# Optimization experiments

Measured on AMD Instinct MI355X. Metric: run time of the kernel, lower is better.

Reference implementation:

```python
import jax, jax.numpy as jnp
import numpy as np

N_FFT = 1024
FREQ = N_FFT // 2 + 1          # 513
FRAMES = 256
WIN_MIN = 10.0                 # max(1, n_fft//100)
WIN_MAX = 1024.0               # n_fft
HOP_MIN = 1.0
HOP_MAX = 256.0
EPS = 1e-12
SIG_LEN = int(HOP_MAX) * FRAMES + N_FFT  # 66560


def setup_inputs() -> dict:
    key = jax.random.key(0)
    k1, k2, k3 = jax.random.split(key, 3)
    x = jax.random.normal(k1, (4, SIG_LEN), dtype=jnp.float32)
    raw_win_length = jax.random.normal(k2, (FREQ,), dtype=jnp.float32)
    raw_hop_length = jax.random.normal(k3, (1,), dtype=jnp.float32)
    return {"x": x, "raw_win_length": raw_win_length, "raw_hop_length": raw_hop_length}


def reference(x, raw_win_length, raw_hop_length):
    B, L = x.shape
    dt = x.dtype
    # sigmoid reparameterization (matches logit init in __init__)
    hop = HOP_MIN + jax.nn.sigmoid(raw_hop_length[0]) * (HOP_MAX - HOP_MIN)      # scalar
    theta = WIN_MIN + jax.nn.sigmoid(raw_win_length) * (WIN_MAX - WIN_MIN)

    # fractional frame positions: integer floor for gather, differentiable frac
    t = jnp.arange(FRAMES, dtype=dt)
    pos = jnp.clip(t * hop, 0.0, float(L - N_FFT))                               # [T]
    idx_floor = jnp.floor(pos).astype(jnp.int32)                                 # [T] (non-diff)
    idx_frac = pos - idx_floor.astype(dt)                                        # [T] (diff: d/dhop = t)

    # unfold: frames[b,t,n] = x[b, idx_floor[t] + n]
    n = jnp.arange(N_FFT)
    frames = x[:, idx_floor[:, None] + n[None, :]]                               # [B,T,N]

    # fractionally-shifted, per-frequency-length hann window: [F,T,N]
    nf = n.astype(dt)
    d = nf[None, :] - (N_FFT - 1) / 2.0 - idx_frac[:, None]                      # [T,N] offset from true center
    th = theta[:, None, None]                                                    # [F,1,1]
    w = jnp.where(jnp.abs(d)[None] <= th / 2.0,
                  0.5 + 0.5 * jnp.cos(2.0 * jnp.pi * d[None] / th),
                  0.0)                                                           # [F,T,N]

    # direct DFT (window varies per freq bin -> no FFT possible)
    k = jnp.arange(FREQ, dtype=dt)
    ang = 2.0 * jnp.pi * k[:, None] * nf[None, :] / N_FFT                        # [F,N]
    re = jnp.einsum('btn,ftn,fn->bft', frames, w, jnp.cos(ang))
    im = -jnp.einsum('btn,ftn,fn->bft', frames, w, jnp.sin(ang))
    stft = jax.lax.complex(re, im)                                               # [B,F,T]
    spec = jnp.abs(stft) + EPS                                                   # magnitude_power = 1
    return spec, stft
```

## Files before the change

kernel.cpp:

```cpp
#include <hip/hip_runtime.h>
#include <math.h>

#define NFFT   1024
#define FREQ   513
#define FRAMES 256
#define SIGLEN 66560
#define NB     4
#define BFT    (NB * FREQ * FRAMES)
#define NWAVE  8
#define NTHR   (64 * NWAVE)
#define NCHUNK 9
#define UNITS  (NCHUNK * FRAMES)

__global__ __launch_bounds__(1024)
void dstft_perm(const float* __restrict__ raw_win, int* __restrict__ perm)
{
    __shared__ float th[FREQ];
    const int tid = threadIdx.x;
    if (tid < FREQ)
        th[tid] = 10.0f + 1014.0f / (1.0f + expf(-raw_win[tid]));
    __syncthreads();
    if (tid < FREQ) {
        const float ti = th[tid];
        int r = 0;
        for (int j = 0; j < FREQ; ++j) {
            const float tj = th[j];
            r += (tj > ti) || (tj == ti && j < tid);
        }
        perm[r] = tid;
    }
}

__device__ __forceinline__ float sigmoid_f32(float v)
{
    if (v >= 0.0f) {
        return 1.0f / (1.0f + expf(-v));
    } else {
        const float e = expf(v);
        return e / (1.0f + e);
    }
}

__device__ __forceinline__ float rfl_f32(float v)
{
    return __int_as_float(__builtin_amdgcn_readfirstlane(__float_as_int(v)));
}

__global__ __launch_bounds__(NTHR)
void dstft_main(const float* __restrict__ x,
                const float* __restrict__ raw_win,
                const float* __restrict__ raw_hop,
                const int* __restrict__ perm,
                float* __restrict__ out, int out_size, int stft_mode)
{
    const int tid  = threadIdx.x;
    const int lane = tid & 63;
    const int q    = tid >> 6;

    __shared__ __align__(16) unsigned char smem[NWAVE * 64 * 9 * 4];
    float4* xlds = reinterpret_cast<float4*>(smem);
    float (*part)[64][9] = reinterpret_cast<float (*)[64][9]>(smem);

    const int u     = (int)blockIdx.x;
    const int chunk = u >> 8;
    const int t     = u & 255;
    const int spos  = chunk * 64 + lane;
    const bool active = (spos < FREQ);

    int f = 0;
    if (active) {
        f = perm ? perm[spos] : spos;
        f = (f < 0) ? 0 : ((f > FREQ - 1) ? (FREQ - 1) : f);
    }
    const float theta = active
        ? (10.0f + sigmoid_f32(raw_win[f]) * 1014.0f)
        : 10.0f;

    float tmaxv = theta;
#pragma unroll
    for (int s = 32; s; s >>= 1)
        tmaxv = fmaxf(tmaxv, __shfl_xor(tmaxv, s, 64));
    const float tmax = rfl_f32(tmaxv);

    const float hop = 1.0f + sigmoid_f32(raw_hop[0]) * 255.0f;
    float pos = (float)t * hop;
    pos = fminf(fmaxf(pos, 0.0f), 65536.0f);
    const float fl   = floorf(pos);
    const int   base = __builtin_amdgcn_readfirstlane((int)fl);
    const float c    = rfl_f32(511.5f + (pos - fl));

    int lo = (int)floorf(c - 0.5f * tmax);
    int hi = (int)ceilf (c + 0.5f * tmax);
    lo = lo > 0 ? lo : 0;
    hi = hi < (NFFT - 1) ? hi : (NFFT - 1);
    int cnt = hi - lo + 1;
    cnt = cnt < 0 ? 0 : (cnt > NFFT ? NFFT : cnt);
    lo  = __builtin_amdgcn_readfirstlane(lo);
    cnt = __builtin_amdgcn_readfirstlane(cnt);

    for (int n = lo + tid; n < lo + cnt; n += NTHR) {
        float4 v;
        v.x = x[base + n];
        v.y = x[base + n + SIGLEN];
        v.z = x[base + n + 2 * SIGLEN];
        v.w = x[base + n + 3 * SIGLEN];
        xlds[n - lo] = v;
    }
    __syncthreads();

    const int s0     = lo + (cnt * q) / NWAVE;
    const int s1     = lo + (cnt * (q + 1)) / NWAVE;
    const int segcnt = s1 - s0;

    const float invth = 1.0f / theta;
    float r = ((float)s0 - c) * invth;

    const float sdr = (float)f * (1.0f / 1024.0f);
    const float cd  = __builtin_amdgcn_cosf(sdr);
    const float sd  = __builtin_amdgcn_sinf(sdr);
    int m0 = (f * s0) & (NFFT - 1);
    m0 = (m0 >= 512) ? (m0 - 1024) : m0;
    const float p0 = (float)m0 * (1.0f / 1024.0f);
    float ca = __builtin_amdgcn_cosf(p0);
    float sa = __builtin_amdgcn_sinf(p0);

    float re0 = 0.f, re1 = 0.f, re2 = 0.f, re3 = 0.f;
    float sm0 = 0.f, sm1 = 0.f, sm2 = 0.f, sm3 = 0.f;

    const float4* __restrict__ xp = &xlds[s0 - lo];
#pragma unroll 4
    for (int i = 0; i < segcnt; ++i) {
        const float rc = __builtin_amdgcn_fmed3f(r, -0.5f, 0.5f);
        const float w  = fmaf(0.5f, __builtin_amdgcn_cosf(rc), 0.5f);
        const float wc  = w * ca;
        const float wsn = w * sa;
        const float4 v = xp[i];
        re0 = fmaf(v.x, wc, re0);  sm0 = fmaf(v.x, wsn, sm0);
        re1 = fmaf(v.y, wc, re1);  sm1 = fmaf(v.y, wsn, sm1);
        re2 = fmaf(v.z, wc, re2);  sm2 = fmaf(v.z, wsn, sm2);
        re3 = fmaf(v.w, wc, re3);  sm3 = fmaf(v.w, wsn, sm3);
        const float nca = fmaf(ca, cd, -(sa * sd));
        const float nsa = fmaf(sa, cd,   ca * sd);
        ca = nca; sa = nsa;
        r += invth;
    }

    __syncthreads();
    part[q][lane][0] = re0;  part[q][lane][1] = re1;
    part[q][lane][2] = re2;  part[q][lane][3] = re3;
    part[q][lane][4] = sm0;  part[q][lane][5] = sm1;
    part[q][lane][6] = sm2;  part[q][lane][7] = sm3;
    __syncthreads();

    if (tid < 256 && active) {
        const int b = tid >> 6;
        float res = 0.f, sms = 0.f;
#pragma unroll
        for (int p = 0; p < NWAVE; ++p) {
            res += part[p][lane][b];
            sms += part[p][lane][4 + b];
        }
        const float re = res;
        const float im = -sms;
        const int idx = b * (FREQ * FRAMES) + f * FRAMES + t;
        if (idx < out_size)
            out[idx] = sqrtf(fmaf(re, re, im * im)) + 1e-12f;
        if (stft_mode == 2) {
            if (BFT + 2 * idx + 1 < out_size) {
                out[BFT + 2 * idx]     = re;
                out[BFT + 2 * idx + 1] = im;
            }
        } else {
            if (BFT + idx < out_size)
                out[BFT + idx] = re;
        }
    }
}

extern "C" void kernel_launch(void* const* d_in, const int* in_sizes, int n_in,
                              void* d_out, int out_size, void* d_ws, size_t ws_size,
                              hipStream_t stream)
{
    const float* x       = (const float*)d_in[0];
    const float* raw_win = (const float*)d_in[1];
    const float* raw_hop = (const float*)d_in[2];
    float* out = (float*)d_out;

    int* perm = nullptr;
    if (d_ws != nullptr && ws_size >= 4096) {
        perm = (int*)d_ws;
        dstft_perm<<<1, 1024, 0, stream>>>(raw_win, perm);
    }
    const int stft_mode = (out_size >= 3 * BFT) ? 2 : 1;
    dstft_main<<<UNITS, NTHR, 0, stream>>>(
        x, raw_win, raw_hop, perm, out, out_size, stft_mode);
}
```

Measured before the change: 58.44 us.

## Process two units per block with prefetch of second unit's samples

Blocks shrink from 8 to 4 waves, and each block now handles two work units, pairing unit u with UNITS-1-u so that heavy and light units share a block. The first three float4 strides of the second unit's samples are loaded into registers before the first unit is computed, so that global load latency overlaps with the first unit's DFT loop. The final reduction now uses all 4 waves, one per batch element. Each wave now iterates over twice as many samples per unit, and register pressure rises from holding the prefetched data.

```diff
diff --git a/kernel.cpp b/kernel.cpp
--- a/kernel.cpp
+++ b/kernel.cpp
@@ -7,10 +7,11 @@
 #define SIGLEN 66560
 #define NB     4
 #define BFT    (NB * FREQ * FRAMES)
-#define NWAVE  8
+#define NWAVE  4
 #define NTHR   (64 * NWAVE)
 #define NCHUNK 9
 #define UNITS  (NCHUNK * FRAMES)
+#define GRID   (UNITS / 2)
 
 __global__ __launch_bounds__(1024)
 void dstft_perm(const float* __restrict__ raw_win, int* __restrict__ perm)
@@ -46,88 +47,80 @@
     return __int_as_float(__builtin_amdgcn_readfirstlane(__float_as_int(v)));
 }
 
-__global__ __launch_bounds__(NTHR)
-void dstft_main(const float* __restrict__ x,
-                const float* __restrict__ raw_win,
-                const float* __restrict__ raw_hop,
-                const int* __restrict__ perm,
-                float* __restrict__ out, int out_size, int stft_mode)
-{
-    const int tid  = threadIdx.x;
-    const int lane = tid & 63;
-    const int q    = tid >> 6;
-
-    __shared__ __align__(16) unsigned char smem[NWAVE * 64 * 9 * 4];
-    float4* xlds = reinterpret_cast<float4*>(smem);
-    float (*part)[64][9] = reinterpret_cast<float (*)[64][9]>(smem);
-
-    const int u     = (int)blockIdx.x;
+struct Unit {
+    int   f;
+    float theta;
+    int   gbase;
+    float c;
+    int   lo, cnt;
+    int   t;
+    bool  active;
+};
+
+__device__ __forceinline__ Unit unit_params(int u, int lane, float hop,
+        const float* __restrict__ raw_win, const int* __restrict__ perm)
+{
+    Unit P;
     const int chunk = u >> 8;
-    const int t     = u & 255;
-    const int spos  = chunk * 64 + lane;
-    const bool active = (spos < FREQ);
-
+    P.t = u & 255;
+    const int spos = chunk * 64 + lane;
+    P.active = (spos < FREQ);
     int f = 0;
-    if (active) {
+    if (P.active) {
         f = perm ? perm[spos] : spos;
         f = (f < 0) ? 0 : ((f > FREQ - 1) ? (FREQ - 1) : f);
     }
-    const float theta = active
-        ? (10.0f + sigmoid_f32(raw_win[f]) * 1014.0f)
-        : 10.0f;
-
-    float tmaxv = theta;
+    P.f = f;
+    P.theta = P.active ? (10.0f + sigmoid_f32(raw_win[f]) * 1014.0f) : 10.0f;
+
+    float tmaxv = P.theta;
 #pragma unroll
     for (int s = 32; s; s >>= 1)
         tmaxv = fmaxf(tmaxv, __shfl_xor(tmaxv, s, 64));
     const float tmax = rfl_f32(tmaxv);
 
-    const float hop = 1.0f + sigmoid_f32(raw_hop[0]) * 255.0f;
-    float pos = (float)t * hop;
+    float pos = (float)P.t * hop;
     pos = fminf(fmaxf(pos, 0.0f), 65536.0f);
-    const float fl   = floorf(pos);
-    const int   base = __builtin_amdgcn_readfirstlane((int)fl);
-    const float c    = rfl_f32(511.5f + (pos - fl));
-
-    int lo = (int)floorf(c - 0.5f * tmax);
-    int hi = (int)ceilf (c + 0.5f * tmax);
+    const float fl = floorf(pos);
+    const int base = __builtin_amdgcn_readfirstlane((int)fl);
+    P.c = rfl_f32(511.5f + (pos - fl));
+
+    int lo = (int)floorf(P.c - 0.5f * tmax);
+    int hi = (int)ceilf (P.c + 0.5f * tmax);
     lo = lo > 0 ? lo : 0;
     hi = hi < (NFFT - 1) ? hi : (NFFT - 1);
     int cnt = hi - lo + 1;
     cnt = cnt < 0 ? 0 : (cnt > NFFT ? NFFT : cnt);
-    lo  = __builtin_amdgcn_readfirstlane(lo);
-    cnt = __builtin_amdgcn_readfirstlane(cnt);
-
-    for (int n = lo + tid; n < lo + cnt; n += NTHR) {
-        float4 v;
-        v.x = x[base + n];
-        v.y = x[base + n + SIGLEN];
-        v.z = x[base + n + 2 * SIGLEN];
-        v.w = x[base + n + 3 * SIGLEN];
-        xlds[n - lo] = v;
-    }
-    __syncthreads();
-
-    const int s0     = lo + (cnt * q) / NWAVE;
-    const int s1     = lo + (cnt * (q + 1)) / NWAVE;
+    P.lo    = __builtin_amdgcn_readfirstlane(lo);
+    P.cnt   = __builtin_amdgcn_readfirstlane(cnt);
+    P.gbase = base + P.lo;
+    return P;
+}
+
+__device__ __forceinline__ void process_unit(const Unit& P, int q, int lane,
+    const float4* __restrict__ xlds, float (*part)[64][9],
+    float* __restrict__ out, int out_size, int stft_mode)
+{
+    const int s0     = P.lo + (P.cnt * q) / NWAVE;
+    const int s1     = P.lo + (P.cnt * (q + 1)) / NWAVE;
     const int segcnt = s1 - s0;
 
-    const float invth = 1.0f / theta;
-    float r = ((float)s0 - c) * invth;
-
-    const float sdr = (float)f * (1.0f / 1024.0f);
+    const float invth = 1.0f / P.theta;
+    float r = ((float)s0 - P.c) * invth;
+
+    const float sdr = (float)P.f * (1.0f / 1024.0f);
     const float cd  = __builtin_amdgcn_cosf(sdr);
     const float sd  = __builtin_amdgcn_sinf(sdr);
-    int m0 = (f * s0) & (NFFT - 1);
+    int m0 = (P.f * s0) & (NFFT - 1);
     m0 = (m0 >= 512) ? (m0 - 1024) : m0;
     const float p0 = (float)m0 * (1.0f / 1024.0f);
     float ca = __builtin_amdgcn_cosf(p0);
     float sa = __builtin_amdgcn_sinf(p0);
 
-    float re0 = 0.f, re1 = 0.f, re2 = 0.f, re3 = 0.f;
-    float sm0 = 0.f, sm1 = 0.f, sm2 = 0.f, sm3 = 0.f;
-
-    const float4* __restrict__ xp = &xlds[s0 - lo];
+    float re0=0.f, re1=0.f, re2=0.f, re3=0.f;
+    float sm0=0.f, sm1=0.f, sm2=0.f, sm3=0.f;
+
+    const float4* __restrict__ xp = &xlds[s0 - P.lo];
 #pragma unroll 4
     for (int i = 0; i < segcnt; ++i) {
         const float rc = __builtin_amdgcn_fmed3f(r, -0.5f, 0.5f);
@@ -152,17 +145,16 @@
     part[q][lane][6] = sm2;  part[q][lane][7] = sm3;
     __syncthreads();
 
-    if (tid < 256 && active) {
-        const int b = tid >> 6;
+    if (P.active) {
         float res = 0.f, sms = 0.f;
 #pragma unroll
         for (int p = 0; p < NWAVE; ++p) {
-            res += part[p][lane][b];
-            sms += part[p][lane][4 + b];
+            res += part[p][lane][q];
+            sms += part[p][lane][4 + q];
         }
         const float re = res;
         const float im = -sms;
-        const int idx = b * (FREQ * FRAMES) + f * FRAMES + t;
+        const int idx = q * (FREQ * FRAMES) + P.f * FRAMES + P.t;
         if (idx < out_size)
             out[idx] = sqrtf(fmaf(re, re, im * im)) + 1e-12f;
         if (stft_mode == 2) {
@@ -177,6 +169,69 @@
     }
 }
 
+__global__ __launch_bounds__(NTHR)
+void dstft_main(const float* __restrict__ x,
+                const float* __restrict__ raw_win,
+                const float* __restrict__ raw_hop,
+                const int* __restrict__ perm,
+                float* __restrict__ out, int out_size, int stft_mode)
+{
+    const int tid  = threadIdx.x;
+    const int lane = tid & 63;
+    const int q    = tid >> 6;
+
+    __shared__ __align__(16) unsigned char smem[NFFT * sizeof(float4)];
+    float4* xlds = reinterpret_cast<float4*>(smem);
+    float (*part)[64][9] = reinterpret_cast<float (*)[64][9]>(smem);
+
+    const float hop = 1.0f + sigmoid_f32(raw_hop[0]) * 255.0f;
+    const int u1 = (int)blockIdx.x;
+    const int u2 = UNITS - 1 - u1;
+
+    const Unit P1 = unit_params(u1, lane, hop, raw_win, perm);
+    const Unit P2 = unit_params(u2, lane, hop, raw_win, perm);
+
+    const int c2m = P2.cnt - 1;
+    int j0 = tid;            j0 = j0 < c2m ? j0 : c2m;
+    int j1 = tid + NTHR;     j1 = j1 < c2m ? j1 : c2m;
+    int j2 = tid + 2*NTHR;   j2 = j2 < c2m ? j2 : c2m;
+    float4 pf0, pf1, pf2;
+    pf0.x = x[P2.gbase + j0];              pf0.y = x[P2.gbase + j0 + SIGLEN];
+    pf0.z = x[P2.gbase + j0 + 2*SIGLEN];   pf0.w = x[P2.gbase + j0 + 3*SIGLEN];
+    pf1.x = x[P2.gbase + j1];              pf1.y = x[P2.gbase + j1 + SIGLEN];
+    pf1.z = x[P2.gbase + j1 + 2*SIGLEN];   pf1.w = x[P2.gbase + j1 + 3*SIGLEN];
+    pf2.x = x[P2.gbase + j2];              pf2.y = x[P2.gbase + j2 + SIGLEN];
+    pf2.z = x[P2.gbase + j2 + 2*SIGLEN];   pf2.w = x[P2.gbase + j2 + 3*SIGLEN];
+
+    for (int n = tid; n < P1.cnt; n += NTHR) {
+        float4 v;
+        v.x = x[P1.gbase + n];
+        v.y = x[P1.gbase + n + SIGLEN];
+        v.z = x[P1.gbase + n + 2 * SIGLEN];
+        v.w = x[P1.gbase + n + 3 * SIGLEN];
+        xlds[n] = v;
+    }
+    __syncthreads();
+
+    process_unit(P1, q, lane, xlds, part, out, out_size, stft_mode);
+
+    __syncthreads();
+    if (tid            < P2.cnt) xlds[tid]            = pf0;
+    if (tid +   NTHR   < P2.cnt) xlds[tid +   NTHR]   = pf1;
+    if (tid + 2*NTHR   < P2.cnt) xlds[tid + 2*NTHR]   = pf2;
+    for (int n = 3*NTHR + tid; n < P2.cnt; n += NTHR) {
+        float4 v;
+        v.x = x[P2.gbase + n];
+        v.y = x[P2.gbase + n + SIGLEN];
+        v.z = x[P2.gbase + n + 2 * SIGLEN];
+        v.w = x[P2.gbase + n + 3 * SIGLEN];
+        xlds[n] = v;
+    }
+    __syncthreads();
+
+    process_unit(P2, q, lane, xlds, part, out, out_size, stft_mode);
+}
+
 extern "C" void kernel_launch(void* const* d_in, const int* in_sizes, int n_in,
                               void* d_out, int out_size, void* d_ws, size_t ws_size,
                               hipStream_t stream)
@@ -192,6 +247,6 @@
         dstft_perm<<<1, 1024, 0, stream>>>(raw_win, perm);
     }
     const int stft_mode = (out_size >= 3 * BFT) ? 2 : 1;
-    dstft_main<<<UNITS, NTHR, 0, stream>>>(
+    dstft_main<<<GRID, NTHR, 0, stream>>>(
         x, raw_win, raw_hop, perm, out, out_size, stft_mode);
 }
```

Result: slower. 63.63 us (+8.9%).

## Halve waves per block, pack complex accumulators into float2 FMA ops

Applied to the files above, without the earlier changes.

Each block now uses 4 waves instead of 8, so every wave handles twice as many samples of the window span, and all four waves take part in the final reduction, one batch each. The inner loop keeps the real and imaginary accumulators and the rotating phasor as 2-wide float vectors so the compiler can emit packed FP32 FMA instructions, which cuts VALU instruction count per sample. Shared memory is resized to cover a full NFFT-long float4 span, fixing a latent overflow when the window span is long. Fewer waves per block means less latency hiding and more serial work per wave.

```diff
diff --git a/kernel.cpp b/kernel.cpp
--- a/kernel.cpp
+++ b/kernel.cpp
@@ -7,10 +7,12 @@
 #define SIGLEN 66560
 #define NB     4
 #define BFT    (NB * FREQ * FRAMES)
-#define NWAVE  8
+#define NWAVE  4
 #define NTHR   (64 * NWAVE)
 #define NCHUNK 9
 #define UNITS  (NCHUNK * FRAMES)
+
+typedef float f32x2 __attribute__((ext_vector_type(2)));
 
 __global__ __launch_bounds__(1024)
 void dstft_perm(const float* __restrict__ raw_win, int* __restrict__ perm)
@@ -57,7 +59,7 @@
     const int lane = tid & 63;
     const int q    = tid >> 6;
 
-    __shared__ __align__(16) unsigned char smem[NWAVE * 64 * 9 * 4];
+    __shared__ __align__(16) unsigned char smem[NFFT * sizeof(float4)];
     float4* xlds = reinterpret_cast<float4*>(smem);
     float (*part)[64][9] = reinterpret_cast<float (*)[64][9]>(smem);
 
@@ -121,48 +123,52 @@
     int m0 = (f * s0) & (NFFT - 1);
     m0 = (m0 >= 512) ? (m0 - 1024) : m0;
     const float p0 = (float)m0 * (1.0f / 1024.0f);
-    float ca = __builtin_amdgcn_cosf(p0);
-    float sa = __builtin_amdgcn_sinf(p0);
-
-    float re0 = 0.f, re1 = 0.f, re2 = 0.f, re3 = 0.f;
-    float sm0 = 0.f, sm1 = 0.f, sm2 = 0.f, sm3 = 0.f;
+
+    f32x2 p;
+    p.x = __builtin_amdgcn_cosf(p0);
+    p.y = __builtin_amdgcn_sinf(p0);
+    const f32x2 cdv = { cd,  cd };
+    const f32x2 sdv = { -sd, sd };
+
+    f32x2 acc0 = {0.f, 0.f}, acc1 = {0.f, 0.f};
+    f32x2 acc2 = {0.f, 0.f}, acc3 = {0.f, 0.f};
 
     const float4* __restrict__ xp = &xlds[s0 - lo];
 #pragma unroll 4
     for (int i = 0; i < segcnt; ++i) {
         const float rc = __builtin_amdgcn_fmed3f(r, -0.5f, 0.5f);
         const float w  = fmaf(0.5f, __builtin_amdgcn_cosf(rc), 0.5f);
-        const float wc  = w * ca;
-        const float wsn = w * sa;
+        const f32x2 w2  = { w, w };
+        const f32x2 wcs = w2 * p;
         const float4 v = xp[i];
-        re0 = fmaf(v.x, wc, re0);  sm0 = fmaf(v.x, wsn, sm0);
-        re1 = fmaf(v.y, wc, re1);  sm1 = fmaf(v.y, wsn, sm1);
-        re2 = fmaf(v.z, wc, re2);  sm2 = fmaf(v.z, wsn, sm2);
-        re3 = fmaf(v.w, wc, re3);  sm3 = fmaf(v.w, wsn, sm3);
-        const float nca = fmaf(ca, cd, -(sa * sd));
-        const float nsa = fmaf(sa, cd,   ca * sd);
-        ca = nca; sa = nsa;
+        const f32x2 v0 = { v.x, v.x }, v1 = { v.y, v.y };
+        const f32x2 v2 = { v.z, v.z }, v3 = { v.w, v.w };
+        acc0 = __builtin_elementwise_fma(v0, wcs, acc0);
+        acc1 = __builtin_elementwise_fma(v1, wcs, acc1);
+        acc2 = __builtin_elementwise_fma(v2, wcs, acc2);
+        acc3 = __builtin_elementwise_fma(v3, wcs, acc3);
+        const f32x2 ps = p.yx;
+        p = __builtin_elementwise_fma(p, cdv, ps * sdv);
         r += invth;
     }
 
     __syncthreads();
-    part[q][lane][0] = re0;  part[q][lane][1] = re1;
-    part[q][lane][2] = re2;  part[q][lane][3] = re3;
-    part[q][lane][4] = sm0;  part[q][lane][5] = sm1;
-    part[q][lane][6] = sm2;  part[q][lane][7] = sm3;
-    __syncthreads();
-
-    if (tid < 256 && active) {
-        const int b = tid >> 6;
+    part[q][lane][0] = acc0.x;  part[q][lane][1] = acc1.x;
+    part[q][lane][2] = acc2.x;  part[q][lane][3] = acc3.x;
+    part[q][lane][4] = acc0.y;  part[q][lane][5] = acc1.y;
+    part[q][lane][6] = acc2.y;  part[q][lane][7] = acc3.y;
+    __syncthreads();
+
+    if (active) {
         float res = 0.f, sms = 0.f;
 #pragma unroll
-        for (int p = 0; p < NWAVE; ++p) {
-            res += part[p][lane][b];
-            sms += part[p][lane][4 + b];
+        for (int pw = 0; pw < NWAVE; ++pw) {
+            res += part[pw][lane][q];
+            sms += part[pw][lane][4 + q];
         }
         const float re = res;
         const float im = -sms;
-        const int idx = b * (FREQ * FRAMES) + f * FRAMES + t;
+        const int idx = q * (FREQ * FRAMES) + f * FRAMES + t;
         if (idx < out_size)
             out[idx] = sqrtf(fmaf(re, re, im * im)) + 1e-12f;
         if (stft_mode == 2) {
```

Measured after the change: 57.22 us. 2.1% less time.
